# Kernel optimization log

Measured on AMD Instinct MI355X. Metric: run time of the kernel, lower is better.

## Reference

```python
import jax, jax.numpy as jnp
import numpy as np

N_NODES = 50000
N_EDGES = 640000
IN_DIM = 128
HID = 128
G_OUT = 128
AX_IN = 64
AX_OUT = 64
OUT_CH = 8
N_GRAPHS = 512


def gcn_conv(x, W, b, src, dst, norm, n_nodes):
    # PyG GCNConv: out = scatter_add(norm * (x W)[src] -> dst) + b
    h = x @ W  # [N, F_out]
    msg = h[src] * norm[:, None]  # [E', F_out]
    return jax.ops.segment_sum(msg, dst, num_segments=n_nodes) + b


def setup_inputs() -> dict:
    key = jax.random.key(0)
    ks = jax.random.split(key, 16)
    inp = {}
    inp["x"] = jax.random.normal(ks[0], (N_NODES, IN_DIM), dtype=jnp.float32)
    inp["edge_index"] = jax.random.randint(ks[1], (2, N_EDGES), 0, N_NODES, dtype=jnp.int64)
    inp["batch"] = jnp.sort(jax.random.randint(ks[2], (N_NODES,), 0, N_GRAPHS, dtype=jnp.int64))
    inp["ax_data"] = jax.random.normal(ks[3], (N_GRAPHS, AX_IN), dtype=jnp.float32)
    def lin(k, fi, fo):
        s = 1.0 / np.sqrt(fi)
        k1, k2 = jax.random.split(k)
        return (jax.random.uniform(k1, (fi, fo), jnp.float32, -s, s),
                jax.random.uniform(k2, (fo,), jnp.float32, -s, s))
    inp["W1"], inp["b1"] = lin(ks[4], IN_DIM, HID)
    inp["W2"], inp["b2"] = lin(ks[5], HID, HID)
    inp["lin1_W"], inp["lin1_b"] = lin(ks[6], HID, G_OUT)
    inp["ax_W"], inp["ax_b"] = lin(ks[7], AX_IN, AX_OUT)
    inp["lin2_W"], inp["lin2_b"] = lin(ks[8], G_OUT + AX_OUT, OUT_CH)
    return inp


def reference(x, edge_index, batch, ax_data, W1, b1, W2, b2, lin1_W, lin1_b, ax_W, ax_b, lin2_W, lin2_b):
    n_nodes = x.shape[0]
    n_graphs = ax_data.shape[0]
    # add self-loops (PyG GCNConv default add_self_loops=True)
    loop = jnp.arange(n_nodes, dtype=edge_index.dtype)
    src = jnp.concatenate([edge_index[0], loop])
    dst = jnp.concatenate([edge_index[1], loop])
    # symmetric normalization D^-1/2 (A+I) D^-1/2
    deg = jax.ops.segment_sum(jnp.ones_like(dst, dtype=x.dtype), dst, num_segments=n_nodes)
    dinv = jax.lax.rsqrt(jnp.maximum(deg, 1.0))  # deg >= 1 with self-loops
    norm = dinv[src] * dinv[dst]  # [E+N]

    h = jax.nn.relu(gcn_conv(x, W1, b1, src, dst, norm, n_nodes))
    h = jax.nn.relu(gcn_conv(h, W2, b2, src, dst, norm, n_nodes))

    # global_mean_pool over batch ids
    sums = jax.ops.segment_sum(h, batch, num_segments=n_graphs)
    cnts = jax.ops.segment_sum(jnp.ones((n_nodes,), h.dtype), batch, num_segments=n_graphs)
    pooled = sums / jnp.maximum(cnts, 1.0)[:, None]  # [G, HID]

    g = pooled @ lin1_W + lin1_b            # [G, G_OUT]
    a = ax_data @ ax_W + ax_b               # [G, AX_OUT]
    z = jnp.concatenate([g, a], axis=1)     # [G, G_OUT+AX_OUT]
    return z @ lin2_W + lin2_b              # [G, OUT_CH]
```

## Files before the change

### kernel.cpp

```cpp
#include <hip/hip_runtime.h>


#define ELLCAP 62
#define BCAP 2048

typedef __attribute__((ext_vector_type(8))) short bf16x8;
typedef __attribute__((ext_vector_type(4))) float f32x4;
typedef __attribute__((ext_vector_type(2))) float f32x2;
typedef __attribute__((ext_vector_type(4))) unsigned int u32x4;

static __device__ __forceinline__ unsigned short f2bf(float f) {
  unsigned u = __float_as_uint(f);
  return (unsigned short)((u + 0x7fffu + ((u >> 16) & 1u)) >> 16);
}
static __device__ __forceinline__ unsigned pack2(float a, float b) {
  return (unsigned)f2bf(a) | ((unsigned)f2bf(b) << 16);
}
static __device__ __forceinline__ unsigned char f2fp8(float v) {
  return (unsigned char)(__builtin_amdgcn_cvt_pk_fp8_f32(v, 0.f, 0, false) & 0xff);
}
static __device__ __forceinline__ unsigned enc2(float a, float b) {
  return __builtin_amdgcn_cvt_pk_fp8_f32(a, b, 0, false) & 0xffffu;
}
static __device__ __forceinline__ void add16(float* a, uint4 h) {
  f32x2 t;
  t = __builtin_amdgcn_cvt_pk_f32_fp8(h.x, false); a[0] += t[0]; a[1] += t[1];
  t = __builtin_amdgcn_cvt_pk_f32_fp8(h.x, true);  a[2] += t[0]; a[3] += t[1];
  t = __builtin_amdgcn_cvt_pk_f32_fp8(h.y, false); a[4] += t[0]; a[5] += t[1];
  t = __builtin_amdgcn_cvt_pk_f32_fp8(h.y, true);  a[6] += t[0]; a[7] += t[1];
  t = __builtin_amdgcn_cvt_pk_f32_fp8(h.z, false); a[8] += t[0]; a[9] += t[1];
  t = __builtin_amdgcn_cvt_pk_f32_fp8(h.z, true);  a[10] += t[0]; a[11] += t[1];
  t = __builtin_amdgcn_cvt_pk_f32_fp8(h.w, false); a[12] += t[0]; a[13] += t[1];
  t = __builtin_amdgcn_cvt_pk_f32_fp8(h.w, true);  a[14] += t[0]; a[15] += t[1];
}
static __device__ __forceinline__ uint4 scale16(uint4 h, float d) {
  f32x2 t; float v[16];
  t = __builtin_amdgcn_cvt_pk_f32_fp8(h.x, false); v[0] = d * t[0]; v[1] = d * t[1];
  t = __builtin_amdgcn_cvt_pk_f32_fp8(h.x, true);  v[2] = d * t[0]; v[3] = d * t[1];
  t = __builtin_amdgcn_cvt_pk_f32_fp8(h.y, false); v[4] = d * t[0]; v[5] = d * t[1];
  t = __builtin_amdgcn_cvt_pk_f32_fp8(h.y, true);  v[6] = d * t[0]; v[7] = d * t[1];
  t = __builtin_amdgcn_cvt_pk_f32_fp8(h.z, false); v[8] = d * t[0]; v[9] = d * t[1];
  t = __builtin_amdgcn_cvt_pk_f32_fp8(h.z, true);  v[10] = d * t[0]; v[11] = d * t[1];
  t = __builtin_amdgcn_cvt_pk_f32_fp8(h.w, false); v[12] = d * t[0]; v[13] = d * t[1];
  t = __builtin_amdgcn_cvt_pk_f32_fp8(h.w, true);  v[14] = d * t[0]; v[15] = d * t[1];
  uint4 r;
  r.x = enc2(v[0], v[1]) | (enc2(v[2], v[3]) << 16);
  r.y = enc2(v[4], v[5]) | (enc2(v[6], v[7]) << 16);
  r.z = enc2(v[8], v[9]) | (enc2(v[10], v[11]) << 16);
  r.w = enc2(v[12], v[13]) | (enc2(v[14], v[15]) << 16);
  return r;
}

__global__ void k_wprep(const float* __restrict__ W1, const float* __restrict__ W2,
                        unsigned short* __restrict__ wt1, unsigned short* __restrict__ wt2,
                        unsigned* __restrict__ gcnt, int nb) {
  int b = blockIdx.x, t = threadIdx.x;
  if (b < 128) {
    int idx = b * 256 + t;
    int w = idx >> 14, r = (idx >> 7) & 127, kk = idx & 127;
    if (w == 0) wt1[r * 128 + kk] = f2bf(W1[kk * 128 + r]);
    else        wt2[r * 128 + kk] = f2bf(W2[kk * 128 + r]);
  } else {
    int i = (b - 128) * 256 + t;
    if (i < nb) gcnt[i * 32] = 0;
  }
}

__global__ __launch_bounds__(256, 4) void k_mega1(
    const float* __restrict__ X, const uint4* __restrict__ WT4,
    unsigned char* __restrict__ H8,
    const int* __restrict__ srcv, const int* __restrict__ dstv,
    unsigned* __restrict__ gcnt, unsigned* __restrict__ packed,
    int E, int M, int NG) {
  __shared__ __align__(16) unsigned short sW[64 * 136];
  __shared__ __align__(16) unsigned short sX[64 * 136];
  __shared__ unsigned sbin[392];
  __shared__ unsigned sbase[392];
  int b = blockIdx.x, t = threadIdx.x;
  if (b < NG) {
    int m0 = b * 64;
    const float4* X4 = (const float4*)X;
#pragma unroll
    for (int r = 0; r < 8; r++) {
      int idx = t + r * 256;
      int rr = idx >> 5, c4 = idx & 31;
      int m = m0 + rr;
      float4 v = make_float4(0.f, 0.f, 0.f, 0.f);
      if (m < M) v = X4[(size_t)m * 32 + c4];
      unsigned short* pp = sX + rr * 136 + c4 * 4;
      *(ushort2*)(pp) = make_ushort2(f2bf(v.x), f2bf(v.y));
      *(ushort2*)(pp + 2) = make_ushort2(f2bf(v.z), f2bf(v.w));
    }
    int lane = t & 63, wv = t >> 6;
    int ln15 = lane & 15, q = lane >> 4;
    int r0 = m0 + wv * 16 + q * 4;
    bf16x8 afrag[4];
#pragma unroll
    for (int half = 0; half < 2; half++) {
      if (half) __syncthreads();
#pragma unroll
      for (int r = 0; r < 4; r++) {
        int idx = t + r * 256;
        int nn = idx >> 4, c8 = idx & 15;
        *(uint4*)(sW + nn * 136 + c8 * 8) = WT4[(half * 64 + nn) * 16 + c8];
      }
      __syncthreads();
      if (half == 0) {
#pragma unroll
        for (int c = 0; c < 4; c++)
          afrag[c] = *(const bf16x8*)(sX + (wv * 16 + ln15) * 136 + c * 32 + q * 8);
      }
#pragma unroll
      for (int jj = 0; jj < 4; jj++) {
        int j = half * 4 + jj;
        f32x4 acc = {0.f, 0.f, 0.f, 0.f};
#pragma unroll
        for (int c = 0; c < 4; c++) {
          bf16x8 bfrag = *(const bf16x8*)(sW + (jj * 16 + ln15) * 136 + c * 32 + q * 8);
          acc = __builtin_amdgcn_mfma_f32_16x16x32_bf16(afrag[c], bfrag, acc, 0, 0, 0);
        }
        int col = j * 16 + ln15;
#pragma unroll
        for (int rr = 0; rr < 4; rr++) {
          int m = r0 + rr;
          if (m < M) H8[(size_t)m * 128 + col] = f2fp8(acc[rr]);
        }
      }
    }
  } else {
    int NB = (M + 127) >> 7;
    int e0 = (b - NG) * BCAP;
    int myS[8], myD[8];
#pragma unroll
    for (int j = 0; j < 8; j++) {
      int e = e0 + t + j * 256;
      if (e < E) { myS[j] = srcv[e]; myD[j] = dstv[e]; } else myD[j] = -1;
    }
    for (int i = t; i < NB; i += 256) sbin[i] = 0;
    __syncthreads();
#pragma unroll
    for (int j = 0; j < 8; j++)
      if (myD[j] >= 0) atomicAdd(&sbin[myD[j] >> 7], 1u);
    __syncthreads();
    for (int i = t; i < NB; i += 256) {
      unsigned c = sbin[i];
      sbase[i] = c ? atomicAdd(&gcnt[i * 32], c) : 0u;
    }
    __syncthreads();
    for (int i = t; i < NB; i += 256) sbin[i] = 0;
    __syncthreads();
#pragma unroll
    for (int j = 0; j < 8; j++)
      if (myD[j] >= 0) {
        int bkt = myD[j] >> 7;
        unsigned r = atomicAdd(&sbin[bkt], 1u);
        unsigned pos = sbase[bkt] + r;
        if (pos < BCAP)
          packed[(size_t)bkt * BCAP + pos] =
              (unsigned)myS[j] | ((unsigned)(myD[j] & 127) << 16);
      }
  }
}

__global__ __launch_bounds__(256) void k_ellbuild(const unsigned* __restrict__ packed,
                                                  const unsigned* __restrict__ gcnt,
                                                  unsigned char* __restrict__ ellb,
                                                  uint4* __restrict__ H8,
                                                  float* __restrict__ dinv,
                                                  int n) {
  __shared__ unsigned short ent[128][ELLCAP];
  __shared__ int ctr[128];
  __shared__ int scnt;
  int b = blockIdx.x, t = threadIdx.x;
  if (t < 128) ctr[t] = 0;
  if (t == 0) scnt = (int)gcnt[b * 32];
  __syncthreads();
  int cnt = scnt; if (cnt > BCAP) cnt = BCAP;
  const unsigned* pk = packed + (size_t)b * BCAP;
  for (int idx = t; idx < cnt; idx += 256) {
    unsigned v = pk[idx];
    int dloc = (int)(v >> 16);
    int slot = atomicAdd(&ctr[dloc], 1);
    if (slot < ELLCAP) ent[dloc][slot] = (unsigned short)(v & 0xffffu);
  }
  __syncthreads();
  int base = b * 128;
#pragma unroll
  for (int p = 0; p < 16; p++) {
    int idx = t + p * 256;
    int i = idx >> 5, u = idx & 31;
    int node = base + i;
    if (node < n) {
      unsigned val;
      if (u == 0) val = (unsigned)ctr[i];
      else {
        int e0 = 2 * u - 2;
        val = (unsigned)ent[i][e0] | ((unsigned)ent[i][e0 + 1] << 16);
      }
      ((unsigned*)ellb)[(size_t)node * 32 + u] = val;
    }
  }
#pragma unroll
  for (int p = 0; p < 4; p++) {
    int idx = t + p * 256;
    int i2 = idx >> 3, kk = idx & 7;
    int node = base + i2;
    if (node < n) {
      float di = rsqrtf((float)(ctr[i2] + 1));
      uint4 h = H8[(size_t)node * 8 + kk];
      H8[(size_t)node * 8 + kk] = scale16(h, di);
      if (kk == 0) dinv[node] = di;
    }
  }
}

#define GLOAD(H, wa, wb, wc, wd, J)                                          \
  {                                                                          \
    int i0_ = (int)((wa) & 0xffffu), i1_ = (int)((wa) >> 16);                \
    int i2_ = (int)((wb) & 0xffffu), i3_ = (int)((wb) >> 16);                \
    int i4_ = (int)((wc) & 0xffffu), i5_ = (int)((wc) >> 16);                \
    int i6_ = (int)((wd) & 0xffffu), i7_ = (int)((wd) >> 16);                \
    if ((J) + 0 >= deg) i0_ = s0;  if ((J) + 1 >= deg) i1_ = s0;             \
    if ((J) + 2 >= deg) i2_ = s0;  if ((J) + 3 >= deg) i3_ = s0;             \
    if ((J) + 4 >= deg) i4_ = s0;  if ((J) + 5 >= deg) i5_ = s0;             \
    if ((J) + 6 >= deg) i6_ = s0;  if ((J) + 7 >= deg) i7_ = s0;             \
    H[0] = Hs[(size_t)i0_ * 8 + k]; H[1] = Hs[(size_t)i1_ * 8 + k];          \
    H[2] = Hs[(size_t)i2_ * 8 + k]; H[3] = Hs[(size_t)i3_ * 8 + k];          \
    H[4] = Hs[(size_t)i4_ * 8 + k]; H[5] = Hs[(size_t)i5_ * 8 + k];          \
    H[6] = Hs[(size_t)i6_ * 8 + k]; H[7] = Hs[(size_t)i7_ * 8 + k];          \
  }
#define CONSUME(H, J)                                                        \
  _Pragma("unroll")                                                          \
  for (int u_ = 0; u_ < 8; u_++)                                             \
    if ((J) + u_ < deg) add16(acc, H[u_]);

__global__ __launch_bounds__(256, 4) void k_agg(const uint4* __restrict__ Hs,
                                                const unsigned char* __restrict__ ellb,
                                                const float* __restrict__ dinv,
                                                const float* __restrict__ bias,
                                                uint4* __restrict__ Ho, int n) {
  int t = threadIdx.x;
  int oct = t >> 3, k = t & 7;
  int i = blockIdx.x * 32 + oct;
  bool valid = i < n;
  int ic = valid ? i : 0;
  const uint4* rp = (const uint4*)(ellb + (size_t)ic * 128);
  uint4 q0 = rp[0], q1 = rp[1], q2 = rp[2], q3 = rp[3];
  uint4 hs = Hs[(size_t)ic * 8 + k];
  float di = dinv[ic];
  int raw = (int)q0.x;
  int deg = raw < ELLCAP ? raw : ELLCAP;
  int s0 = (int)(q0.y & 0xffffu);
  float acc[16];
#pragma unroll
  for (int r = 0; r < 16; r++) acc[r] = 0.f;
  uint4 hA[8], hB[8];
  if (deg > 0)  GLOAD(hA, q0.y, q0.z, q0.w, q1.x, 0);
  if (deg > 8)  GLOAD(hB, q1.y, q1.z, q1.w, q2.x, 8);
  add16(acc, hs);
  if (deg > 0)  CONSUME(hA, 0);
  if (deg > 16) GLOAD(hA, q2.y, q2.z, q2.w, q3.x, 16);
  if (deg > 8)  CONSUME(hB, 8);
  if (deg > 24) {
    const unsigned* wp = (const unsigned*)(ellb + (size_t)ic * 128 + 4);
    {
      unsigned wa = wp[12], wb = wp[13], wc = wp[14], wd = wp[15];
      GLOAD(hB, wa, wb, wc, wd, 24);
    }
    if (deg > 16) CONSUME(hA, 16);
    CONSUME(hB, 24);
    for (int j = 32; j < deg; j += 8) {
      unsigned wa = wp[j / 2], wb = wp[j / 2 + 1], wc = wp[j / 2 + 2], wd = wp[j / 2 + 3];
      GLOAD(hA, wa, wb, wc, wd, j);
      CONSUME(hA, j);
    }
  } else {
    if (deg > 16) CONSUME(hA, 16);
  }
  if (valid) {
    const float4* B4 = (const float4*)bias;
    float o[16];
#pragma unroll
    for (int m4 = 0; m4 < 4; m4++) {
      float4 bb = B4[k * 4 + m4];
      o[m4 * 4 + 0] = fmaxf(bb.x + di * acc[m4 * 4 + 0], 0.f);
      o[m4 * 4 + 1] = fmaxf(bb.y + di * acc[m4 * 4 + 1], 0.f);
      o[m4 * 4 + 2] = fmaxf(bb.z + di * acc[m4 * 4 + 2], 0.f);
      o[m4 * 4 + 3] = fmaxf(bb.w + di * acc[m4 * 4 + 3], 0.f);
    }
    u32x4 r0, r1;
    r0[0] = pack2(o[0], o[1]);   r0[1] = pack2(o[2], o[3]);
    r0[2] = pack2(o[4], o[5]);   r0[3] = pack2(o[6], o[7]);
    r1[0] = pack2(o[8], o[9]);   r1[1] = pack2(o[10], o[11]);
    r1[2] = pack2(o[12], o[13]); r1[3] = pack2(o[14], o[15]);
    __builtin_nontemporal_store(r0, (u32x4*)&Ho[(size_t)i * 16 + 2 * k]);
    __builtin_nontemporal_store(r1, (u32x4*)&Ho[(size_t)i * 16 + 2 * k + 1]);
  }
}

__global__ __launch_bounds__(256, 2) void k_gemm2(const unsigned short* __restrict__ Xb,
                                                  const uint4* __restrict__ WT4,
                                                  const float* __restrict__ dinv,
                                                  unsigned char* __restrict__ H8, int M) {
  __shared__ __align__(16) unsigned short sW[128 * 136];
  __shared__ __align__(16) unsigned short sX[64 * 136];
  int tid = threadIdx.x;
  int m0 = blockIdx.x * 64;
#pragma unroll
  for (int r = 0; r < 8; r++) {
    int idx = tid + r * 256;
    int nn = idx >> 4, c8 = idx & 15;
    *(uint4*)(sW + nn * 136 + c8 * 8) = WT4[idx];
  }
  const uint4* X4 = (const uint4*)Xb;
#pragma unroll
  for (int r = 0; r < 4; r++) {
    int idx = tid + r * 256;
    int rr = idx >> 4, c8 = idx & 15;
    int m = m0 + rr;
    uint4 v = make_uint4(0u, 0u, 0u, 0u);
    if (m < M) v = X4[(size_t)m * 16 + c8];
    *(uint4*)(sX + rr * 136 + c8 * 8) = v;
  }
  __syncthreads();
  int lane = tid & 63, wv = tid >> 6;
  int ln15 = lane & 15, q = lane >> 4;
  bf16x8 afrag[4];
#pragma unroll
  for (int c = 0; c < 4; c++)
    afrag[c] = *(const bf16x8*)(sX + (wv * 16 + ln15) * 136 + c * 32 + q * 8);
  int r0 = m0 + wv * 16 + q * 4;
  float dv[4];
#pragma unroll
  for (int rr = 0; rr < 4; rr++) dv[rr] = (r0 + rr < M) ? dinv[r0 + rr] : 0.f;
#pragma unroll
  for (int j = 0; j < 8; j++) {
    f32x4 acc = {0.f, 0.f, 0.f, 0.f};
#pragma unroll
    for (int c = 0; c < 4; c++) {
      bf16x8 bfrag = *(const bf16x8*)(sW + (j * 16 + ln15) * 136 + c * 32 + q * 8);
      acc = __builtin_amdgcn_mfma_f32_16x16x32_bf16(afrag[c], bfrag, acc, 0, 0, 0);
    }
    int col = j * 16 + ln15;
#pragma unroll
    for (int rr = 0; rr < 4; rr++) {
      int m = r0 + rr;
      if (m < M) H8[(size_t)m * 128 + col] = f2fp8(dv[rr] * acc[rr]);
    }
  }
}

__global__ void k_poolhead(const unsigned short* __restrict__ Hb,
                           const int* __restrict__ bat, const float* __restrict__ axd,
                           const float* __restrict__ l1W, const float* __restrict__ l1b,
                           const float* __restrict__ axW, const float* __restrict__ axb,
                           const float* __restrict__ l2W, const float* __restrict__ l2b,
                           float* __restrict__ out, int n) {
  int g = blockIdx.x, t = threadIdx.x;
  __shared__ int sb[2];
  __shared__ float p[128];
  __shared__ float a[64];
  __shared__ float z[192];
  if (t < 2) {
    int target = g + t;
    int lo = 0, hi = n;
    while (lo < hi) {
      int mid = (lo + hi) >> 1;
      if (bat[mid] < target) lo = mid + 1; else hi = mid;
    }
    sb[t] = lo;
  }
  __syncthreads();
  int s = sb[0], e = sb[1];
  int c = e - s; if (c < 1) c = 1;
  float inv = 1.f / (float)c;
  if (t < 128) {
    float s0 = 0.f, s1 = 0.f, s2 = 0.f, s3 = 0.f;
    float s4 = 0.f, s5 = 0.f, s6 = 0.f, s7 = 0.f;
    int r = s;
    for (; r + 8 <= e; r += 8) {
      s0 += __uint_as_float(((unsigned)Hb[(size_t)(r + 0) * 128 + t]) << 16);
      s1 += __uint_as_float(((unsigned)Hb[(size_t)(r + 1) * 128 + t]) << 16);
      s2 += __uint_as_float(((unsigned)Hb[(size_t)(r + 2) * 128 + t]) << 16);
      s3 += __uint_as_float(((unsigned)Hb[(size_t)(r + 3) * 128 + t]) << 16);
      s4 += __uint_as_float(((unsigned)Hb[(size_t)(r + 4) * 128 + t]) << 16);
      s5 += __uint_as_float(((unsigned)Hb[(size_t)(r + 5) * 128 + t]) << 16);
      s6 += __uint_as_float(((unsigned)Hb[(size_t)(r + 6) * 128 + t]) << 16);
      s7 += __uint_as_float(((unsigned)Hb[(size_t)(r + 7) * 128 + t]) << 16);
    }
    for (; r < e; r++)
      s0 += __uint_as_float(((unsigned)Hb[(size_t)r * 128 + t]) << 16);
    p[t] = (((s0 + s1) + (s2 + s3)) + ((s4 + s5) + (s6 + s7))) * inv;
  } else {
    a[t - 128] = axd[g * 64 + (t - 128)];
  }
  __syncthreads();
  if (t < 128) {
    float a0 = 0.f, a1 = 0.f, a2 = 0.f, a3 = 0.f;
#pragma unroll 8
    for (int kk = 0; kk < 128; kk += 4) {
      a0 += p[kk + 0] * l1W[(kk + 0) * 128 + t];
      a1 += p[kk + 1] * l1W[(kk + 1) * 128 + t];
      a2 += p[kk + 2] * l1W[(kk + 2) * 128 + t];
      a3 += p[kk + 3] * l1W[(kk + 3) * 128 + t];
    }
    z[t] = l1b[t] + (a0 + a1) + (a2 + a3);
  } else {
    int j = t - 128;
    float a0 = 0.f, a1 = 0.f, a2 = 0.f, a3 = 0.f;
#pragma unroll 8
    for (int kk = 0; kk < 64; kk += 4) {
      a0 += a[kk + 0] * axW[(kk + 0) * 64 + j];
      a1 += a[kk + 1] * axW[(kk + 1) * 64 + j];
      a2 += a[kk + 2] * axW[(kk + 2) * 64 + j];
      a3 += a[kk + 3] * axW[(kk + 3) * 64 + j];
    }
    z[128 + j] = axb[j] + (a0 + a1) + (a2 + a3);
  }
  __syncthreads();
  if (t < 8) {
    float a0 = 0.f, a1 = 0.f, a2 = 0.f, a3 = 0.f;
#pragma unroll 8
    for (int kk = 0; kk < 192; kk += 4) {
      a0 += z[kk + 0] * l2W[(kk + 0) * 8 + t];
      a1 += z[kk + 1] * l2W[(kk + 1) * 8 + t];
      a2 += z[kk + 2] * l2W[(kk + 2) * 8 + t];
      a3 += z[kk + 3] * l2W[(kk + 3) * 8 + t];
    }
    out[g * 8 + t] = l2b[t] + (a0 + a1) + (a2 + a3);
  }
}

extern "C" void kernel_launch(void* const* d_in, const int* in_sizes, int n_in,
                              void* d_out, int out_size, void* d_ws, size_t ws_size,
                              hipStream_t stream) {
  const float* x   = (const float*)d_in[0];
  const int*   ei  = (const int*)d_in[1];
  const int*   bat = (const int*)d_in[2];
  const float* axd = (const float*)d_in[3];
  const float* W1  = (const float*)d_in[4];
  const float* b1  = (const float*)d_in[5];
  const float* W2  = (const float*)d_in[6];
  const float* b2  = (const float*)d_in[7];
  const float* l1W = (const float*)d_in[8];
  const float* l1b = (const float*)d_in[9];
  const float* axW = (const float*)d_in[10];
  const float* axb = (const float*)d_in[11];
  const float* l2W = (const float*)d_in[12];
  const float* l2b = (const float*)d_in[13];
  float* out = (float*)d_out;

  int n = in_sizes[0] / 128;
  int E = in_sizes[1] / 2;
  int G = in_sizes[3] / 64;
  (void)G;
  int NB = (n + 127) / 128;

  unsigned char* w = (unsigned char*)d_ws;
  unsigned char*  h8    = w;                     w += (size_t)n * 128;
  unsigned short* habuf = (unsigned short*)w;    w += (size_t)n * 128 * 2;
  unsigned short* wt1   = (unsigned short*)w;    w += 16384 * 2;
  unsigned short* wt2   = (unsigned short*)w;    w += 16384 * 2;
  unsigned char*  ellb  = w;                     w += (size_t)n * 128;
  float*    dinv   = (float*)w;                  w += (size_t)n * 4;
  unsigned* gcnt   = (unsigned*)w;               w += (size_t)NB * 128;
  unsigned* packed = (unsigned*)w;               w += (size_t)NB * BCAP * 4;

  const int* srcv = ei;
  const int* dstv = ei + E;
  int NG = (n + 63) / 64;
  int NPB = (E + BCAP - 1) / BCAP;
  int GZ = (NB + 255) / 256;

  k_wprep<<<128 + GZ, 256, 0, stream>>>(W1, W2, wt1, wt2, gcnt, NB);
  k_mega1<<<NG + NPB, 256, 0, stream>>>(x, (const uint4*)wt1, h8, srcv, dstv,
                                        gcnt, packed, E, n, NG);
  k_ellbuild<<<NB, 256, 0, stream>>>(packed, gcnt, ellb, (uint4*)h8, dinv, n);
  k_agg<<<(n + 31) / 32, 256, 0, stream>>>((const uint4*)h8, ellb, dinv, b1,
                                           (uint4*)habuf, n);
  k_gemm2<<<NG, 256, 0, stream>>>(habuf, (const uint4*)wt2, dinv, h8, n);
  k_agg<<<(n + 31) / 32, 256, 0, stream>>>((const uint4*)h8, ellb, dinv, b2,
                                           (uint4*)habuf, n);
  k_poolhead<<<512, 192, 0, stream>>>(habuf, bat, axd, l1W, l1b, axW, axb,
                                      l2W, l2b, out, n);
}
```

Baseline: 193.0 us.

## Fuse layer-1 aggregation with layer-2 GEMM via shared-memory tile

Merges the first GCN aggregation kernel and the second-layer GEMM into one kernel. Each block aggregates 64 nodes (two passes of 32), writes the bf16 results straight into shared memory, then runs MFMA against W2 and emits fp8 features into a new separate buffer. This drops one kernel launch and the global round trip of the bf16 intermediate, since the GEMM input no longer has to be written and reread. In exchange, occupancy is lower because of the larger shared-memory footprint and launch bounds of 3. The gather latency now also sits serially before the MFMA phase within each block, and the second aggregation's stores lose their nontemporal hint.

After: 182.7 us. 5.3% less time.

```diff
diff --git a/kernel.cpp b/kernel.cpp
--- a/kernel.cpp
+++ b/kernel.cpp
@@ -7,7 +7,6 @@
 typedef __attribute__((ext_vector_type(8))) short bf16x8;
 typedef __attribute__((ext_vector_type(4))) float f32x4;
 typedef __attribute__((ext_vector_type(2))) float f32x2;
-typedef __attribute__((ext_vector_type(4))) unsigned int u32x4;
 
 static __device__ __forceinline__ unsigned short f2bf(float f) {
   unsigned u = __float_as_uint(f);
@@ -234,6 +233,108 @@
   for (int u_ = 0; u_ < 8; u_++)                                             \
     if ((J) + u_ < deg) add16(acc, H[u_]);
 
+#define AGG_BODY(i, o)                                                       \
+  {                                                                          \
+    bool valid = (i) < n;                                                    \
+    int ic = valid ? (i) : 0;                                                \
+    const uint4* rp = (const uint4*)(ellb + (size_t)ic * 128);               \
+    uint4 q0 = rp[0], q1 = rp[1], q2 = rp[2], q3 = rp[3];                    \
+    uint4 hs = Hs[(size_t)ic * 8 + k];                                       \
+    float di = dinv[ic];                                                     \
+    int raw = (int)q0.x;                                                     \
+    int deg = raw < ELLCAP ? raw : ELLCAP;                                   \
+    int s0 = (int)(q0.y & 0xffffu);                                          \
+    float acc[16];                                                           \
+    _Pragma("unroll") for (int r = 0; r < 16; r++) acc[r] = 0.f;             \
+    uint4 hA[8], hB[8];                                                      \
+    if (deg > 0)  GLOAD(hA, q0.y, q0.z, q0.w, q1.x, 0);                      \
+    if (deg > 8)  GLOAD(hB, q1.y, q1.z, q1.w, q2.x, 8);                      \
+    add16(acc, hs);                                                          \
+    if (deg > 0)  CONSUME(hA, 0);                                            \
+    if (deg > 16) GLOAD(hA, q2.y, q2.z, q2.w, q3.x, 16);                     \
+    if (deg > 8)  CONSUME(hB, 8);                                            \
+    if (deg > 24) {                                                          \
+      const unsigned* wp = (const unsigned*)(ellb + (size_t)ic * 128 + 4);   \
+      { unsigned wa = wp[12], wb = wp[13], wc = wp[14], wd = wp[15];         \
+        GLOAD(hB, wa, wb, wc, wd, 24); }                                     \
+      if (deg > 16) CONSUME(hA, 16);                                         \
+      CONSUME(hB, 24);                                                       \
+      for (int j = 32; j < deg; j += 8) {                                    \
+        unsigned wa = wp[j / 2], wb = wp[j / 2 + 1];                         \
+        unsigned wc = wp[j / 2 + 2], wd = wp[j / 2 + 3];                     \
+        GLOAD(hA, wa, wb, wc, wd, j);                                        \
+        CONSUME(hA, j);                                                      \
+      }                                                                      \
+    } else {                                                                 \
+      if (deg > 16) CONSUME(hA, 16);                                         \
+    }                                                                        \
+    const float4* B4 = (const float4*)bias;                                  \
+    _Pragma("unroll") for (int m4 = 0; m4 < 4; m4++) {                       \
+      float4 bb = B4[k * 4 + m4];                                            \
+      o[m4 * 4 + 0] = valid ? fmaxf(bb.x + di * acc[m4 * 4 + 0], 0.f) : 0.f; \
+      o[m4 * 4 + 1] = valid ? fmaxf(bb.y + di * acc[m4 * 4 + 1], 0.f) : 0.f; \
+      o[m4 * 4 + 2] = valid ? fmaxf(bb.z + di * acc[m4 * 4 + 2], 0.f) : 0.f; \
+      o[m4 * 4 + 3] = valid ? fmaxf(bb.w + di * acc[m4 * 4 + 3], 0.f) : 0.f; \
+    }                                                                        \
+  }
+
+__global__ __launch_bounds__(256, 3) void k_agg1g2(
+    const uint4* __restrict__ Hs, const unsigned char* __restrict__ ellb,
+    const float* __restrict__ dinv, const float* __restrict__ bias,
+    const uint4* __restrict__ WT4, unsigned char* __restrict__ H8, int n) {
+  __shared__ __align__(16) unsigned short sX[64 * 136];
+  __shared__ __align__(16) unsigned short sW[128 * 136];
+  int t = threadIdx.x;
+  int oct = t >> 3, k = t & 7;
+  int m0 = blockIdx.x * 64;
+#pragma unroll
+  for (int h = 0; h < 2; h++) {
+    int i = m0 + h * 32 + oct;
+    float o[16];
+    AGG_BODY(i, o);
+    unsigned short* pp = sX + (h * 32 + oct) * 136 + k * 16;
+    uint4 w0, w1;
+    w0.x = pack2(o[0], o[1]);   w0.y = pack2(o[2], o[3]);
+    w0.z = pack2(o[4], o[5]);   w0.w = pack2(o[6], o[7]);
+    w1.x = pack2(o[8], o[9]);   w1.y = pack2(o[10], o[11]);
+    w1.z = pack2(o[12], o[13]); w1.w = pack2(o[14], o[15]);
+    *(uint4*)(pp) = w0;
+    *(uint4*)(pp + 8) = w1;
+  }
+#pragma unroll
+  for (int r = 0; r < 8; r++) {
+    int idx = t + r * 256;
+    int nn = idx >> 4, c8 = idx & 15;
+    *(uint4*)(sW + nn * 136 + c8 * 8) = WT4[idx];
+  }
+  __syncthreads();
+  int lane = t & 63, wv = t >> 6;
+  int ln15 = lane & 15, q = lane >> 4;
+  bf16x8 afrag[4];
+#pragma unroll
+  for (int c = 0; c < 4; c++)
+    afrag[c] = *(const bf16x8*)(sX + (wv * 16 + ln15) * 136 + c * 32 + q * 8);
+  int r0 = m0 + wv * 16 + q * 4;
+  float dv[4];
+#pragma unroll
+  for (int rr = 0; rr < 4; rr++) dv[rr] = (r0 + rr < n) ? dinv[r0 + rr] : 0.f;
+#pragma unroll
+  for (int j = 0; j < 8; j++) {
+    f32x4 acc2 = {0.f, 0.f, 0.f, 0.f};
+#pragma unroll
+    for (int c = 0; c < 4; c++) {
+      bf16x8 bfrag = *(const bf16x8*)(sW + (j * 16 + ln15) * 136 + c * 32 + q * 8);
+      acc2 = __builtin_amdgcn_mfma_f32_16x16x32_bf16(afrag[c], bfrag, acc2, 0, 0, 0);
+    }
+    int col = j * 16 + ln15;
+#pragma unroll
+    for (int rr = 0; rr < 4; rr++) {
+      int m = r0 + rr;
+      if (m < n) H8[(size_t)m * 128 + col] = f2fp8(dv[rr] * acc2[rr]);
+    }
+  }
+}
+
 __global__ __launch_bounds__(256, 4) void k_agg(const uint4* __restrict__ Hs,
                                                 const unsigned char* __restrict__ ellb,
                                                 const float* __restrict__ dinv,
@@ -242,111 +343,16 @@
   int t = threadIdx.x;
   int oct = t >> 3, k = t & 7;
   int i = blockIdx.x * 32 + oct;
-  bool valid = i < n;
-  int ic = valid ? i : 0;
-  const uint4* rp = (const uint4*)(ellb + (size_t)ic * 128);
-  uint4 q0 = rp[0], q1 = rp[1], q2 = rp[2], q3 = rp[3];
-  uint4 hs = Hs[(size_t)ic * 8 + k];
-  float di = dinv[ic];
-  int raw = (int)q0.x;
-  int deg = raw < ELLCAP ? raw : ELLCAP;
-  int s0 = (int)(q0.y & 0xffffu);
-  float acc[16];
-#pragma unroll
-  for (int r = 0; r < 16; r++) acc[r] = 0.f;
-  uint4 hA[8], hB[8];
-  if (deg > 0)  GLOAD(hA, q0.y, q0.z, q0.w, q1.x, 0);
-  if (deg > 8)  GLOAD(hB, q1.y, q1.z, q1.w, q2.x, 8);
-  add16(acc, hs);
-  if (deg > 0)  CONSUME(hA, 0);
-  if (deg > 16) GLOAD(hA, q2.y, q2.z, q2.w, q3.x, 16);
-  if (deg > 8)  CONSUME(hB, 8);
-  if (deg > 24) {
-    const unsigned* wp = (const unsigned*)(ellb + (size_t)ic * 128 + 4);
-    {
-      unsigned wa = wp[12], wb = wp[13], wc = wp[14], wd = wp[15];
-      GLOAD(hB, wa, wb, wc, wd, 24);
-    }
-    if (deg > 16) CONSUME(hA, 16);
-    CONSUME(hB, 24);
-    for (int j = 32; j < deg; j += 8) {
-      unsigned wa = wp[j / 2], wb = wp[j / 2 + 1], wc = wp[j / 2 + 2], wd = wp[j / 2 + 3];
-      GLOAD(hA, wa, wb, wc, wd, j);
-      CONSUME(hA, j);
-    }
-  } else {
-    if (deg > 16) CONSUME(hA, 16);
-  }
-  if (valid) {
-    const float4* B4 = (const float4*)bias;
-    float o[16];
-#pragma unroll
-    for (int m4 = 0; m4 < 4; m4++) {
-      float4 bb = B4[k * 4 + m4];
-      o[m4 * 4 + 0] = fmaxf(bb.x + di * acc[m4 * 4 + 0], 0.f);
-      o[m4 * 4 + 1] = fmaxf(bb.y + di * acc[m4 * 4 + 1], 0.f);
-      o[m4 * 4 + 2] = fmaxf(bb.z + di * acc[m4 * 4 + 2], 0.f);
-      o[m4 * 4 + 3] = fmaxf(bb.w + di * acc[m4 * 4 + 3], 0.f);
-    }
-    u32x4 r0, r1;
-    r0[0] = pack2(o[0], o[1]);   r0[1] = pack2(o[2], o[3]);
-    r0[2] = pack2(o[4], o[5]);   r0[3] = pack2(o[6], o[7]);
-    r1[0] = pack2(o[8], o[9]);   r1[1] = pack2(o[10], o[11]);
-    r1[2] = pack2(o[12], o[13]); r1[3] = pack2(o[14], o[15]);
-    __builtin_nontemporal_store(r0, (u32x4*)&Ho[(size_t)i * 16 + 2 * k]);
-    __builtin_nontemporal_store(r1, (u32x4*)&Ho[(size_t)i * 16 + 2 * k + 1]);
-  }
-}
-
-__global__ __launch_bounds__(256, 2) void k_gemm2(const unsigned short* __restrict__ Xb,
-                                                  const uint4* __restrict__ WT4,
-                                                  const float* __restrict__ dinv,
-                                                  unsigned char* __restrict__ H8, int M) {
-  __shared__ __align__(16) unsigned short sW[128 * 136];
-  __shared__ __align__(16) unsigned short sX[64 * 136];
-  int tid = threadIdx.x;
-  int m0 = blockIdx.x * 64;
-#pragma unroll
-  for (int r = 0; r < 8; r++) {
-    int idx = tid + r * 256;
-    int nn = idx >> 4, c8 = idx & 15;
-    *(uint4*)(sW + nn * 136 + c8 * 8) = WT4[idx];
-  }
-  const uint4* X4 = (const uint4*)Xb;
-#pragma unroll
-  for (int r = 0; r < 4; r++) {
-    int idx = tid + r * 256;
-    int rr = idx >> 4, c8 = idx & 15;
-    int m = m0 + rr;
-    uint4 v = make_uint4(0u, 0u, 0u, 0u);
-    if (m < M) v = X4[(size_t)m * 16 + c8];
-    *(uint4*)(sX + rr * 136 + c8 * 8) = v;
-  }
-  __syncthreads();
-  int lane = tid & 63, wv = tid >> 6;
-  int ln15 = lane & 15, q = lane >> 4;
-  bf16x8 afrag[4];
-#pragma unroll
-  for (int c = 0; c < 4; c++)
-    afrag[c] = *(const bf16x8*)(sX + (wv * 16 + ln15) * 136 + c * 32 + q * 8);
-  int r0 = m0 + wv * 16 + q * 4;
-  float dv[4];
-#pragma unroll
-  for (int rr = 0; rr < 4; rr++) dv[rr] = (r0 + rr < M) ? dinv[r0 + rr] : 0.f;
-#pragma unroll
-  for (int j = 0; j < 8; j++) {
-    f32x4 acc = {0.f, 0.f, 0.f, 0.f};
-#pragma unroll
-    for (int c = 0; c < 4; c++) {
-      bf16x8 bfrag = *(const bf16x8*)(sW + (j * 16 + ln15) * 136 + c * 32 + q * 8);
-      acc = __builtin_amdgcn_mfma_f32_16x16x32_bf16(afrag[c], bfrag, acc, 0, 0, 0);
-    }
-    int col = j * 16 + ln15;
-#pragma unroll
-    for (int rr = 0; rr < 4; rr++) {
-      int m = r0 + rr;
-      if (m < M) H8[(size_t)m * 128 + col] = f2fp8(dv[rr] * acc[rr]);
-    }
+  float o[16];
+  AGG_BODY(i, o);
+  if (i < n) {
+    uint4 r0, r1;
+    r0.x = pack2(o[0], o[1]);   r0.y = pack2(o[2], o[3]);
+    r0.z = pack2(o[4], o[5]);   r0.w = pack2(o[6], o[7]);
+    r1.x = pack2(o[8], o[9]);   r1.y = pack2(o[10], o[11]);
+    r1.z = pack2(o[12], o[13]); r1.w = pack2(o[14], o[15]);
+    Ho[(size_t)i * 16 + 2 * k] = r0;
+    Ho[(size_t)i * 16 + 2 * k + 1] = r1;
   }
 }
 
@@ -458,6 +464,7 @@
 
   unsigned char* w = (unsigned char*)d_ws;
   unsigned char*  h8    = w;                     w += (size_t)n * 128;
+  unsigned char*  h8b   = w;                     w += (size_t)n * 128;
   unsigned short* habuf = (unsigned short*)w;    w += (size_t)n * 128 * 2;
   unsigned short* wt1   = (unsigned short*)w;    w += 16384 * 2;
   unsigned short* wt2   = (unsigned short*)w;    w += 16384 * 2;
@@ -476,10 +483,9 @@
   k_mega1<<<NG + NPB, 256, 0, stream>>>(x, (const uint4*)wt1, h8, srcv, dstv,
                                         gcnt, packed, E, n, NG);
   k_ellbuild<<<NB, 256, 0, stream>>>(packed, gcnt, ellb, (uint4*)h8, dinv, n);
-  k_agg<<<(n + 31) / 32, 256, 0, stream>>>((const uint4*)h8, ellb, dinv, b1,
-                                           (uint4*)habuf, n);
-  k_gemm2<<<NG, 256, 0, stream>>>(habuf, (const uint4*)wt2, dinv, h8, n);
-  k_agg<<<(n + 31) / 32, 256, 0, stream>>>((const uint4*)h8, ellb, dinv, b2,
+  k_agg1g2<<<NG, 256, 0, stream>>>((const uint4*)h8, ellb, dinv, b1,
+                                   (const uint4*)wt2, h8b, n);
+  k_agg<<<(n + 31) / 32, 256, 0, stream>>>((const uint4*)h8b, ellb, dinv, b2,
                                            (uint4*)habuf, n);
   k_poolhead<<<512, 192, 0, stream>>>(habuf, bat, axd, l1W, l1b, axW, axb,
                                       l2W, l2b, out, n);
```
